# Kernel optimization log

Measured on AMD Instinct MI355X. Metric: run time of the kernel, lower is better.

## Reference

```python
import jax, jax.numpy as jnp
import numpy as np

# norse LIFParameters defaults with v_th overridden to 0.23
DT = 1e-3
TAU_SYN_INV = 200.0   # 1/5e-3
TAU_MEM_INV = 100.0   # 1/1e-2
V_TH = 0.23
ENC_V_TH = 1.0        # encoder uses default LIFParameters (v_th=1.0)
SEQ_LEN = 24
HIDDEN = 256
N_CLASSES = 10


def heaviside(x):
    return (x > 0).astype(x.dtype)


def encode(x):
    """ConstantCurrentLIFEncoder: lif_current_encoder over SEQ_LEN steps. x: [B, F] -> [T, B, F] spikes."""
    def step(v, _):
        v = v + DT * TAU_MEM_INV * (x - v)          # dv = dt*tau_mem_inv*((v_leak - v) + I)
        z = heaviside(v - ENC_V_TH)
        v = (1.0 - z) * v                            # reset to v_reset = 0
        return v, z
    _, zs = jax.lax.scan(step, jnp.zeros_like(x), None, length=SEQ_LEN)
    return zs


def lif_ff_step(inp, v, i):
    """norse lif_feed_forward_step: decay v with old i, decay i, spike, reset, then add input to i."""
    v_dec = v + DT * TAU_MEM_INV * (i - v)           # v_leak = 0
    i_dec = i * (1.0 - DT * TAU_SYN_INV)
    z = heaviside(v_dec - V_TH)
    v_new = (1.0 - z) * v_dec                        # v_reset = 0
    i_new = i_dec + inp
    return z, v_new, i_new


def setup_inputs() -> dict:
    key = jax.random.key(0)
    ks = jax.random.split(key, 8)
    B, F = 4096, 1024
    def lin(k, fan_in, fan_out):
        bound = 1.0 / np.sqrt(fan_in)
        kw, kb = jax.random.split(k)
        W = jax.random.uniform(kw, (fan_out, fan_in), jnp.float32, -bound, bound)
        b = jax.random.uniform(kb, (fan_out,), jnp.float32, -bound, bound)
        return W, b
    x = jax.random.normal(ks[0], (B, F), jnp.float32)
    W1, b1 = lin(ks[1], F, HIDDEN)
    W2, b2 = lin(ks[2], HIDDEN, HIDDEN)
    W3, b3 = lin(ks[3], HIDDEN, HIDDEN)
    Wli = jax.random.normal(ks[4], (N_CLASSES, HIDDEN), jnp.float32) * np.sqrt(2.0 / HIDDEN)
    return {"x": x, "W1": W1, "b1": b1, "W2": W2, "b2": b2, "W3": W3, "b3": b3, "Wli": Wli}


def reference(x, W1, b1, W2, b2, W3, b3, Wli):
    # dropout layers are identity in eval mode
    enc = encode(x)                                   # [T, B, F]
    B = x.shape[0]
    z2 = lambda d: jnp.zeros((B, d), x.dtype)
    carry0 = (z2(HIDDEN), z2(HIDDEN), z2(HIDDEN), z2(HIDDEN), z2(HIDDEN), z2(HIDDEN),
              z2(N_CLASSES), z2(N_CLASSES))
    def step(c, z):
        v1, i1, v2, i2, v3, i3, vo, io = c
        o1, v1, i1 = lif_ff_step(z @ W1.T + b1, v1, i1)
        o2, v2, i2 = lif_ff_step(o1 @ W2.T + b2, v2, i2)
        o2 = o2 + o1                                  # residual
        o3, v3, i3 = lif_ff_step(o2 @ W3.T + b3, v3, i3)
        o3 = o3 + o2                                  # residual
        # LILinearCell li_step: v from old i, i decays then accumulates W @ input (no bias)
        vo = vo + DT * TAU_MEM_INV * (io - vo)
        io = io * (1.0 - DT * TAU_SYN_INV) + o3 @ Wli.T
        return (v1, i1, v2, i2, v3, i3, vo, io), vo
    _, voltages = jax.lax.scan(step, carry0, enc)     # [T, B, n_classes]
    return voltages[-1]                               # decode = last timestep
```

## Files before the change

### kernel.cpp

```cpp
#include <hip/hip_runtime.h>
#include <hip/hip_bf16.h>

#define FEAT   1024
#define HID    256
#define TSTEPS 24
#define NCLS   10

typedef unsigned int u32;
typedef unsigned long long u64;
typedef unsigned short u16;
typedef float v2f __attribute__((ext_vector_type(2)));

constexpr int OFF_W1T  = 0;
constexpr int OFF_W2T  = OFF_W1T + 1025*HID;
constexpr int OFF_W3T  = OFF_W2T + 257*HID;
constexpr int OFF_WLI  = OFF_W3T + 257*HID;
constexpr int OFF_B1   = OFF_WLI + NCLS*HID;
constexpr int OFF_B2   = OFF_B1 + HID;
constexpr int OFF_B3   = OFF_B2 + HID;

struct CoefT { float c[TSTEPS]; };
constexpr CoefT make_coef() {
    CoefT r{};
    double c = 0.0, p9 = 1.0;
    r.c[TSTEPS-1] = 0.0f;
    for (int u = TSTEPS-1; u > 0; u--) {
        c = 0.8 * c + 0.1 * p9;
        p9 *= 0.9;
        r.c[u-1] = (float)c;
    }
    return r;
}
__device__ constexpr CoefT COEF = make_coef();

__device__ __forceinline__ u32 rfl(u32 v) {
    return (u32)__builtin_amdgcn_readfirstlane((int)v);
}

__device__ __forceinline__ u32 detect_bf16(const void* __restrict__ x, u32 lane) {
    float v = __bfloat162float(((const __hip_bfloat16*)x)[lane]);
    u64 bad = __ballot(!(fabsf(v) < 100.0f));
    return bad == 0ull ? 1u : 0u;
}

__device__ __forceinline__ float rd_any(const void* p, int idx, u32 isbf) {
    return isbf ? __bfloat162float(((const __hip_bfloat16*)p)[idx])
                : ((const float*)p)[idx];
}

__device__ __forceinline__ float4 rd4(const void* p, int i, u32 isbf) {
    if (isbf) {
        const u32* q = (const u32*)p;
        u32 a = q[i >> 1], b = q[(i >> 1) + 1];
        float4 r;
        r.x = __uint_as_float(a << 16); r.y = __uint_as_float(a & 0xffff0000u);
        r.z = __uint_as_float(b << 16); r.w = __uint_as_float(b & 0xffff0000u);
        return r;
    }
    return ((const float4*)p)[i >> 2];
}

__global__ __launch_bounds__(256) void prep_k(const void* __restrict__ x,
        const void* W1, const void* W2, const void* W3, const void* Wli,
        const void* b1, const void* b2, const void* b3, float* __restrict__ ws) {
    const u32 isbf = detect_bf16(x, threadIdx.x & 63);
    const u32 t = threadIdx.x;
    int b = blockIdx.x;

    if (b == 384) {
        for (u32 e = t; e < NCLS*HID; e += 256) ws[OFF_WLI + e] = rd_any(Wli, e, isbf);
        ws[OFF_B1 + t] = rd_any(b1, t, isbf);
        ws[OFF_B2 + t] = rd_any(b2, t, isbf);
        ws[OFF_B3 + t] = rd_any(b3, t, isbf);
        ws[OFF_W1T + 1024*HID + t] = 0.f;
        ws[OFF_W2T + 256*HID + t] = 0.f;
        ws[OFF_W3T + 256*HID + t] = 0.f;
        return;
    }

    const void* src; float* dst; int srcW, h0, f0;
    if (b < 256)      { src = W1; dst = ws + OFF_W1T; srcW = FEAT; h0 = (b >> 5) * 32; f0 = (b & 31) * 32; }
    else if (b < 320) { int tb = b - 256; src = W2; dst = ws + OFF_W2T; srcW = HID; h0 = (tb >> 3) * 32; f0 = (tb & 7) * 32; }
    else              { int tb = b - 320; src = W3; dst = ws + OFF_W3T; srcW = HID; h0 = (tb >> 3) * 32; f0 = (tb & 7) * 32; }

    __shared__ float sm[32 * 36];
    {
        u32 r = t >> 3, c4 = (t & 7) * 4;
        float4 w = rd4(src, (h0 + r) * srcW + f0 + c4, isbf);
        *(float4*)&sm[r * 36 + c4] = w;
    }
    __syncthreads();
    {
        u32 f = t >> 3, h4 = (t & 7) * 4;
        float4 o;
        o.x = sm[(h4 + 0) * 36 + f];
        o.y = sm[(h4 + 1) * 36 + f];
        o.z = sm[(h4 + 2) * 36 + f];
        o.w = sm[(h4 + 3) * 36 + f];
        *(float4*)&dst[(size_t)(f0 + f) * HID + h0 + h4] = o;
    }
}

__device__ __forceinline__ u32 mbcnt64(u64 m) {
    return __builtin_amdgcn_mbcnt_hi((u32)(m >> 32),
           __builtin_amdgcn_mbcnt_lo((u32)m, 0u));
}


__device__ __forceinline__ u32 build_listE(u16* list, u32 lm, u32 lane) {
    u32 cnt = (u32)__builtin_popcount(lm);
    u32 pos = 0, n = 0;
    #pragma unroll
    for (int b = 0; b < 5; b++) {
        u64 B = __ballot(((cnt >> b) & 1u) != 0);
        pos += mbcnt64(B) << b;
        n += ((u32)__builtin_popcountll(B)) << b;
    }
    while (lm) {
        u32 j = (u32)__builtin_ctz(lm); lm &= lm - 1;
        list[pos++] = (u16)((lane << 4) + j);
    }
    u32 np = (n + 1u) & ~1u;
    if (lane == 0 && np != n) list[n] = (u16)1024;
    return np;
}

__device__ __forceinline__ u32 build_listZ(u16* list, u32 lm, u32 start, u32 lane) {
    u32 cnt = (u32)__builtin_popcount(lm);
    u64 B0 = __ballot((cnt & 1u) != 0);
    u64 B1 = __ballot((cnt & 2u) != 0);
    u64 B2 = __ballot((cnt & 4u) != 0);
    u32 pos = start + mbcnt64(B0) + 2u*mbcnt64(B1) + 4u*mbcnt64(B2);
    u32 n = start + (u32)__builtin_popcountll(B0) + 2u*(u32)__builtin_popcountll(B1)
          + 4u*(u32)__builtin_popcountll(B2);
    while (lm) {
        u32 j = (u32)__builtin_ctz(lm); lm &= lm - 1;
        list[pos++] = (u16)((lane << 2) + j);
    }
    u32 np = (n + 1u) & ~1u;
    if (lane == 0 && np != n) list[n] = (u16)256;
    return np;
}

#define GADD(AA, BB, V) do { AA += (v2f){(V).x, (V).y}; BB += (v2f){(V).z, (V).w}; } while (0)

__device__ __forceinline__ void gather(v2f& A, v2f& B, const float* __restrict__ Wt,
                                       const u16* __restrict__ list, u32 np, u32 lane16) {
    const char* __restrict__ base = (const char*)Wt;
    u32 c = 0;
    for (; c + 8 <= np; c += 8) {
        uint4 d = *(const uint4*)(list + c);
        u32 w0 = rfl(d.x), w1 = rfl(d.y), w2 = rfl(d.z), w3 = rfl(d.w);
        const float4 v0 = *(const float4*)(base + ((w0 & 0xffffu) << 10) + lane16);
        const float4 v1 = *(const float4*)(base + ((w0 >> 16)     << 10) + lane16);
        const float4 v2 = *(const float4*)(base + ((w1 & 0xffffu) << 10) + lane16);
        const float4 v3 = *(const float4*)(base + ((w1 >> 16)     << 10) + lane16);
        const float4 v4 = *(const float4*)(base + ((w2 & 0xffffu) << 10) + lane16);
        const float4 v5 = *(const float4*)(base + ((w2 >> 16)     << 10) + lane16);
        const float4 v6 = *(const float4*)(base + ((w3 & 0xffffu) << 10) + lane16);
        const float4 v7 = *(const float4*)(base + ((w3 >> 16)     << 10) + lane16);
        GADD(A, B, v0); GADD(A, B, v1); GADD(A, B, v2); GADD(A, B, v3);
        GADD(A, B, v4); GADD(A, B, v5); GADD(A, B, v6); GADD(A, B, v7);
    }
    for (; c < np; c += 2) {
        u32 d = rfl(*(const u32*)(list + c));
        const float4 v0 = *(const float4*)(base + ((d & 0xffffu) << 10) + lane16);
        const float4 v1 = *(const float4*)(base + ((d >> 16)     << 10) + lane16);
        GADD(A, B, v0); GADD(A, B, v1);
    }
}

__device__ __forceinline__ void gather_dual(v2f& A2, v2f& B2, v2f& A3, v2f& B3,
        const float* __restrict__ W2t, const float* __restrict__ W3t,
        const u16* __restrict__ list, u32 np, u32 lane16) {
    const char* __restrict__ p2 = (const char*)W2t;
    const char* __restrict__ p3 = (const char*)W3t;
    u32 c = 0;
    for (; c + 4 <= np; c += 4) {
        uint2 d = *(const uint2*)(list + c);
        u32 w0 = rfl(d.x), w1 = rfl(d.y);
        u32 o0 = (w0 & 0xffffu) << 10, o1 = (w0 >> 16) << 10;
        u32 o2 = (w1 & 0xffffu) << 10, o3 = (w1 >> 16) << 10;
        const float4 a0 = *(const float4*)(p2 + o0 + lane16);
        const float4 a1 = *(const float4*)(p2 + o1 + lane16);
        const float4 a2 = *(const float4*)(p2 + o2 + lane16);
        const float4 a3 = *(const float4*)(p2 + o3 + lane16);
        const float4 c0 = *(const float4*)(p3 + o0 + lane16);
        const float4 c1 = *(const float4*)(p3 + o1 + lane16);
        const float4 c2 = *(const float4*)(p3 + o2 + lane16);
        const float4 c3 = *(const float4*)(p3 + o3 + lane16);
        GADD(A2, B2, a0); GADD(A2, B2, a1); GADD(A2, B2, a2); GADD(A2, B2, a3);
        GADD(A3, B3, c0); GADD(A3, B3, c1); GADD(A3, B3, c2); GADD(A3, B3, c3);
    }
    for (; c < np; c += 2) {
        u32 d = rfl(*(const u32*)(list + c));
        u32 o0 = (d & 0xffffu) << 10, o1 = (d >> 16) << 10;
        const float4 a0 = *(const float4*)(p2 + o0 + lane16);
        const float4 a1 = *(const float4*)(p2 + o1 + lane16);
        const float4 c0 = *(const float4*)(p3 + o0 + lane16);
        const float4 c1 = *(const float4*)(p3 + o1 + lane16);
        GADD(A2, B2, a0); GADD(A2, B2, a1);
        GADD(A3, B3, c0); GADD(A3, B3, c1);
    }
}

__global__ __launch_bounds__(64) void snn_k(const void* __restrict__ xin,
                                            const float* __restrict__ ws,
                                            void* __restrict__ out) {
    const u32 lane = threadIdx.x;
    const int row  = blockIdx.x;
    const u32 lane16 = lane * 16;
    const u32 isbf = detect_bf16(xin, lane);

    const float* __restrict__ W1T = ws + OFF_W1T;
    const float* __restrict__ W2T = ws + OFF_W2T;
    const float* __restrict__ W3T = ws + OFF_W3T;
    const float* __restrict__ WLI = ws + OFF_WLI;

    __shared__ u32 sched[12 * 64];
    __shared__ __align__(16) u16 lE[1032];
    __shared__ __align__(16) u16 lL[520];

    {
        float xv[16];
        if (isbf) {
            const uint4* xp = (const uint4*)((const u16*)xin + (size_t)row*FEAT + lane*16);
            uint4 A = xp[0], B = xp[1];
            u32 w[8] = {A.x, A.y, A.z, A.w, B.x, B.y, B.z, B.w};
            #pragma unroll
            for (int i = 0; i < 8; i++) {
                xv[2*i]   = __uint_as_float(w[i] << 16);
                xv[2*i+1] = __uint_as_float(w[i] & 0xffff0000u);
            }
        } else {
            const float4* xp = (const float4*)((const float*)xin + (size_t)row*FEAT + lane*16);
            float4 A = xp[0], B = xp[1], C = xp[2], D = xp[3];
            float tmp[16] = {A.x,A.y,A.z,A.w,B.x,B.y,B.z,B.w,C.x,C.y,C.z,C.w,D.x,D.y,D.z,D.w};
            #pragma unroll
            for (int i = 0; i < 16; i++) xv[i] = tmp[i];
        }
        u32 smreg[12];
        #pragma unroll
        for (int i = 0; i < 12; i++) smreg[i] = 0;
        #pragma unroll
        for (int j = 0; j < 16; j++) {
            float v = 0.f;
            #pragma unroll
            for (int t = 0; t < TSTEPS; t++) {
                v = v + 0.1f * (xv[j] - v);
                bool z = v > 1.0f;
                v = z ? 0.0f : v;
                if (z) smreg[t >> 1] |= 1u << (((t & 1) << 4) + j);
            }
        }
        #pragma unroll
        for (int i = 0; i < 12; i++) sched[i * 64 + lane] = smreg[i];
    }

    float v1[4], i1[4], v2[4], i2[4], v3[4], i3[4], g[4];
    #pragma unroll
    for (int k = 0; k < 4; k++) {
        v1[k]=0.f; i1[k]=0.f; v2[k]=0.f; i2[k]=0.f; v3[k]=0.f; i3[k]=0.f; g[k]=0.f;
    }
    const u32 lane4 = lane * 4;
    const float4 b1v = *(const float4*)(ws + OFF_B1 + lane4);
    const float4 b2v = *(const float4*)(ws + OFF_B2 + lane4);
    const float4 b3v = *(const float4*)(ws + OFF_B3 + lane4);

    u32 pairreg = 0;
    for (int t = 0; t < TSTEPS; t++) {
        if ((t & 1) == 0) pairreg = sched[(t >> 1) * 64 + lane];
        const u32 lmE = (t & 1) ? (pairreg >> 16) : (pairreg & 0xffffu);

        v2f accA = {b1v.x, b1v.y}, accB = {b1v.z, b1v.w};
        if (__ballot(lmE != 0u)) {
            u32 npE = build_listE(lE, lmE, lane);
            gather(accA, accB, W1T, lE, npE, lane16);
        }
        float a1[4] = {accA.x, accA.y, accB.x, accB.y};

        float o1v[4]; u32 lm1 = 0;
        #pragma unroll
        for (int kk = 0; kk < 4; kk++) {
            float vd = v1[kk] + 0.1f * (i1[kk] - v1[kk]);
            i1[kk] = i1[kk] * 0.8f;
            bool z = vd > 0.23f;
            v1[kk] = z ? 0.0f : vd;
            i1[kk] = i1[kk] + a1[kk];
            o1v[kk] = z ? 1.0f : 0.0f;
            lm1 |= (z ? 1u : 0u) << kk;
        }

        v2f acc2A = {b2v.x, b2v.y}, acc2B = {b2v.z, b2v.w};
        v2f acc3A = {b3v.x, b3v.y}, acc3B = {b3v.z, b3v.w};
        u32 np1 = 0;
        if (__ballot(lm1 != 0u)) {
            np1 = build_listZ(lL, lm1, 0u, lane);
            gather_dual(acc2A, acc2B, acc3A, acc3B, W2T, W3T, lL, np1, lane16);
        }
        float a2[4] = {acc2A.x, acc2A.y, acc2B.x, acc2B.y};

        float o2v[4]; u32 lm2 = 0;
        #pragma unroll
        for (int kk = 0; kk < 4; kk++) {
            float vd = v2[kk] + 0.1f * (i2[kk] - v2[kk]);
            i2[kk] = i2[kk] * 0.8f;
            bool z = vd > 0.23f;
            v2[kk] = z ? 0.0f : vd;
            i2[kk] = i2[kk] + a2[kk];
            o2v[kk] = (z ? 1.0f : 0.0f) + o1v[kk];
            lm2 |= (z ? 1u : 0u) << kk;
        }

        if (__ballot(lm2 != 0u)) {
            u32 np2 = build_listZ(lL, lm2, np1, lane);
            gather(acc3A, acc3B, W3T, lL + np1, np2 - np1, lane16);
        }
        float a3[4] = {acc3A.x, acc3A.y, acc3B.x, acc3B.y};

        const float cf = COEF.c[t];
        #pragma unroll
        for (int kk = 0; kk < 4; kk++) {
            float vd = v3[kk] + 0.1f * (i3[kk] - v3[kk]);
            i3[kk] = i3[kk] * 0.8f;
            bool z = vd > 0.23f;
            v3[kk] = z ? 0.0f : vd;
            i3[kk] = i3[kk] + a3[kk];
            float o3 = (z ? 1.0f : 0.0f) + o2v[kk];
            g[kk] += cf * o3;
        }
    }

    float s[NCLS];
    #pragma unroll
    for (int c = 0; c < NCLS; c++) {
        const float4 w = *(const float4*)(WLI + c*HID + lane4);
        float p = g[0]*w.x + g[1]*w.y + g[2]*w.z + g[3]*w.w;
        #pragma unroll
        for (int d = 32; d > 0; d >>= 1) p += __shfl_xor(p, d, 64);
        s[c] = p;
    }
    if (lane == 0) {
        if (isbf) {
            __hip_bfloat16* o = (__hip_bfloat16*)out + (size_t)row*NCLS;
            #pragma unroll
            for (int c = 0; c < NCLS; c++) o[c] = __float2bfloat16(s[c]);
        } else {
            float* o = (float*)out + (size_t)row*NCLS;
            #pragma unroll
            for (int c = 0; c < NCLS; c++) o[c] = s[c];
        }
    }
}

extern "C" void kernel_launch(void* const* d_in, const int* in_sizes, int n_in,
                              void* d_out, int out_size, void* d_ws, size_t ws_size,
                              hipStream_t stream) {
    const void* x   = d_in[0];
    const void* W1  = d_in[1];
    const void* b1  = d_in[2];
    const void* W2  = d_in[3];
    const void* b2  = d_in[4];
    const void* W3  = d_in[5];
    const void* b3  = d_in[6];
    const void* Wli = d_in[7];
    float* ws = (float*)d_ws;
    const int batch = in_sizes[0] / FEAT;

    prep_k<<<385, 256, 0, stream>>>(x, W1, W2, W3, Wli, b1, b2, b3, ws);
    snn_k<<<batch, 64, 0, stream>>>(x, ws, d_out);
}
```

Measured before the change: 144.1 us.

## Split each batch row across two wavefronts with K-split gathers and LDS reduction

Each block now runs two wavefronts per batch row. Each wave handles half of the input features or hidden spikes (a K-split) and accumulates partial sums over all 256 outputs. The two waves exchange and sum their partials through shared memory with a __syncthreads at each layer, and each wave then owns 2 of the 4 outputs per lane for the LIF state update. The aim is to halve the per-wave serial gather latency and raise parallelism, at the cost of three block barriers per timestep and extra LDS traffic.

Result: slower. 228.3 us (+58.4%).

```diff
diff --git a/kernel.cpp b/kernel.cpp
--- a/kernel.cpp
+++ b/kernel.cpp
@@ -107,35 +107,33 @@
 }
 
 
-__device__ __forceinline__ u32 build_listE(u16* list, u32 lm, u32 lane) {
+__device__ __forceinline__ u32 build_listE8(u16* list, u32 lm, u32 lane, u32 colbase) {
     u32 cnt = (u32)__builtin_popcount(lm);
     u32 pos = 0, n = 0;
     #pragma unroll
-    for (int b = 0; b < 5; b++) {
+    for (int b = 0; b < 4; b++) {
         u64 B = __ballot(((cnt >> b) & 1u) != 0);
         pos += mbcnt64(B) << b;
         n += ((u32)__builtin_popcountll(B)) << b;
     }
     while (lm) {
         u32 j = (u32)__builtin_ctz(lm); lm &= lm - 1;
-        list[pos++] = (u16)((lane << 4) + j);
+        list[pos++] = (u16)(colbase + (lane << 3) + j);
     }
     u32 np = (n + 1u) & ~1u;
     if (lane == 0 && np != n) list[n] = (u16)1024;
     return np;
 }
 
-__device__ __forceinline__ u32 build_listZ(u16* list, u32 lm, u32 start, u32 lane) {
+__device__ __forceinline__ u32 build_listZ2(u16* list, u32 lm, u32 start, u32 lane, u32 kbase) {
     u32 cnt = (u32)__builtin_popcount(lm);
     u64 B0 = __ballot((cnt & 1u) != 0);
     u64 B1 = __ballot((cnt & 2u) != 0);
-    u64 B2 = __ballot((cnt & 4u) != 0);
-    u32 pos = start + mbcnt64(B0) + 2u*mbcnt64(B1) + 4u*mbcnt64(B2);
-    u32 n = start + (u32)__builtin_popcountll(B0) + 2u*(u32)__builtin_popcountll(B1)
-          + 4u*(u32)__builtin_popcountll(B2);
+    u32 pos = start + mbcnt64(B0) + 2u*mbcnt64(B1);
+    u32 n = start + (u32)__builtin_popcountll(B0) + 2u*(u32)__builtin_popcountll(B1);
     while (lm) {
         u32 j = (u32)__builtin_ctz(lm); lm &= lm - 1;
-        list[pos++] = (u16)((lane << 2) + j);
+        list[pos++] = (u16)((lane << 2) + kbase + j);
     }
     u32 np = (n + 1u) & ~1u;
     if (lane == 0 && np != n) list[n] = (u16)256;
@@ -204,12 +202,15 @@
     }
 }
 
-__global__ __launch_bounds__(64) void snn_k(const void* __restrict__ xin,
-                                            const float* __restrict__ ws,
-                                            void* __restrict__ out) {
-    const u32 lane = threadIdx.x;
+__global__ __launch_bounds__(128, 8) void snn_k(const void* __restrict__ xin,
+                                                const float* __restrict__ ws,
+                                                void* __restrict__ out) {
+    const u32 tid  = threadIdx.x;
+    const u32 w    = tid >> 6;
+    const u32 lane = tid & 63;
     const int row  = blockIdx.x;
     const u32 lane16 = lane * 16;
+    const u32 k0 = w << 1;
     const u32 isbf = detect_bf16(xin, lane);
 
     const float* __restrict__ W1T = ws + OFF_W1T;
@@ -217,71 +218,82 @@
     const float* __restrict__ W3T = ws + OFF_W3T;
     const float* __restrict__ WLI = ws + OFF_WLI;
 
-    __shared__ u32 sched[12 * 64];
-    __shared__ __align__(16) u16 lE[1032];
-    __shared__ __align__(16) u16 lL[520];
+    __shared__ u32 sched[6 * 128];
+    __shared__ __align__(16) u16 lE[2][512];
+    __shared__ __align__(16) u16 lL[2][264];
+    __shared__ v2f exb[3][2][64];
+    __shared__ float redsm[2][NCLS];
 
     {
-        float xv[16];
+        float xv[8];
         if (isbf) {
-            const uint4* xp = (const uint4*)((const u16*)xin + (size_t)row*FEAT + lane*16);
-            uint4 A = xp[0], B = xp[1];
-            u32 w[8] = {A.x, A.y, A.z, A.w, B.x, B.y, B.z, B.w};
+            const u16* xb = (const u16*)xin + (size_t)row * FEAT;
+            uint4 A = *(const uint4*)(xb + tid * 8);
+            u32 wd[4] = {A.x, A.y, A.z, A.w};
             #pragma unroll
-            for (int i = 0; i < 8; i++) {
-                xv[2*i]   = __uint_as_float(w[i] << 16);
-                xv[2*i+1] = __uint_as_float(w[i] & 0xffff0000u);
+            for (int i = 0; i < 4; i++) {
+                xv[2*i]   = __uint_as_float(wd[i] << 16);
+                xv[2*i+1] = __uint_as_float(wd[i] & 0xffff0000u);
             }
         } else {
-            const float4* xp = (const float4*)((const float*)xin + (size_t)row*FEAT + lane*16);
-            float4 A = xp[0], B = xp[1], C = xp[2], D = xp[3];
-            float tmp[16] = {A.x,A.y,A.z,A.w,B.x,B.y,B.z,B.w,C.x,C.y,C.z,C.w,D.x,D.y,D.z,D.w};
-            #pragma unroll
-            for (int i = 0; i < 16; i++) xv[i] = tmp[i];
-        }
-        u32 smreg[12];
-        #pragma unroll
-        for (int i = 0; i < 12; i++) smreg[i] = 0;
-        #pragma unroll
-        for (int j = 0; j < 16; j++) {
+            const float* xf = (const float*)xin + (size_t)row * FEAT;
+            float4 A = ((const float4*)xf)[tid * 2];
+            float4 B = ((const float4*)xf)[tid * 2 + 1];
+            xv[0]=A.x; xv[1]=A.y; xv[2]=A.z; xv[3]=A.w;
+            xv[4]=B.x; xv[5]=B.y; xv[6]=B.z; xv[7]=B.w;
+        }
+        u32 smreg[6];
+        #pragma unroll
+        for (int i = 0; i < 6; i++) smreg[i] = 0;
+        #pragma unroll
+        for (int j = 0; j < 8; j++) {
             float v = 0.f;
             #pragma unroll
             for (int t = 0; t < TSTEPS; t++) {
                 v = v + 0.1f * (xv[j] - v);
                 bool z = v > 1.0f;
                 v = z ? 0.0f : v;
-                if (z) smreg[t >> 1] |= 1u << (((t & 1) << 4) + j);
+                if (z) smreg[t >> 2] |= 1u << (((t & 3) << 3) + j);
             }
         }
         #pragma unroll
-        for (int i = 0; i < 12; i++) sched[i * 64 + lane] = smreg[i];
-    }
-
-    float v1[4], i1[4], v2[4], i2[4], v3[4], i3[4], g[4];
+        for (int i = 0; i < 6; i++) sched[i * 128 + tid] = smreg[i];
+    }
+
+    float v1[2], i1[2], v2_[2], i2[2], v3[2], i3[2], g[2];
     #pragma unroll
-    for (int k = 0; k < 4; k++) {
-        v1[k]=0.f; i1[k]=0.f; v2[k]=0.f; i2[k]=0.f; v3[k]=0.f; i3[k]=0.f; g[k]=0.f;
+    for (int k = 0; k < 2; k++) {
+        v1[k]=0.f; i1[k]=0.f; v2_[k]=0.f; i2[k]=0.f; v3[k]=0.f; i3[k]=0.f; g[k]=0.f;
     }
     const u32 lane4 = lane * 4;
-    const float4 b1v = *(const float4*)(ws + OFF_B1 + lane4);
-    const float4 b2v = *(const float4*)(ws + OFF_B2 + lane4);
-    const float4 b3v = *(const float4*)(ws + OFF_B3 + lane4);
-
-    u32 pairreg = 0;
+    float4 b1v = *(const float4*)(ws + OFF_B1 + lane4);
+    float4 b2v = *(const float4*)(ws + OFF_B2 + lane4);
+    float4 b3v = *(const float4*)(ws + OFF_B3 + lane4);
+    if (w) {
+        b1v = make_float4(0.f,0.f,0.f,0.f);
+        b2v = make_float4(0.f,0.f,0.f,0.f);
+        b3v = make_float4(0.f,0.f,0.f,0.f);
+    }
+    const u32 colbaseE = w << 9;
+
+    u32 curw = 0;
     for (int t = 0; t < TSTEPS; t++) {
-        if ((t & 1) == 0) pairreg = sched[(t >> 1) * 64 + lane];
-        const u32 lmE = (t & 1) ? (pairreg >> 16) : (pairreg & 0xffffu);
+        if ((t & 3) == 0) curw = sched[(t >> 2) * 128 + tid];
+        const u32 lmE = (curw >> ((t & 3) << 3)) & 0xffu;
 
         v2f accA = {b1v.x, b1v.y}, accB = {b1v.z, b1v.w};
         if (__ballot(lmE != 0u)) {
-            u32 npE = build_listE(lE, lmE, lane);
-            gather(accA, accB, W1T, lE, npE, lane16);
-        }
-        float a1[4] = {accA.x, accA.y, accB.x, accB.y};
-
-        float o1v[4]; u32 lm1 = 0;
-        #pragma unroll
-        for (int kk = 0; kk < 4; kk++) {
+            u32 npE = build_listE8(lE[w], lmE, lane, colbaseE);
+            gather(accA, accB, W1T, lE[w], npE, lane16);
+        }
+        exb[0][w][lane] = w ? accA : accB;
+        __syncthreads();
+        v2f own1 = (w ? accB : accA) + exb[0][w ^ 1][lane];
+
+        float a1[2] = {own1.x, own1.y};
+        float o1v[2]; u32 lm1 = 0;
+        #pragma unroll
+        for (int kk = 0; kk < 2; kk++) {
             float vd = v1[kk] + 0.1f * (i1[kk] - v1[kk]);
             i1[kk] = i1[kk] * 0.8f;
             bool z = vd > 0.23f;
@@ -295,32 +307,38 @@
         v2f acc3A = {b3v.x, b3v.y}, acc3B = {b3v.z, b3v.w};
         u32 np1 = 0;
         if (__ballot(lm1 != 0u)) {
-            np1 = build_listZ(lL, lm1, 0u, lane);
-            gather_dual(acc2A, acc2B, acc3A, acc3B, W2T, W3T, lL, np1, lane16);
-        }
-        float a2[4] = {acc2A.x, acc2A.y, acc2B.x, acc2B.y};
-
-        float o2v[4]; u32 lm2 = 0;
-        #pragma unroll
-        for (int kk = 0; kk < 4; kk++) {
-            float vd = v2[kk] + 0.1f * (i2[kk] - v2[kk]);
+            np1 = build_listZ2(lL[w], lm1, 0u, lane, k0);
+            gather_dual(acc2A, acc2B, acc3A, acc3B, W2T, W3T, lL[w], np1, lane16);
+        }
+        exb[1][w][lane] = w ? acc2A : acc2B;
+        __syncthreads();
+        v2f own2 = (w ? acc2B : acc2A) + exb[1][w ^ 1][lane];
+
+        float a2[2] = {own2.x, own2.y};
+        float o2v[2]; u32 lm2 = 0;
+        #pragma unroll
+        for (int kk = 0; kk < 2; kk++) {
+            float vd = v2_[kk] + 0.1f * (i2[kk] - v2_[kk]);
             i2[kk] = i2[kk] * 0.8f;
             bool z = vd > 0.23f;
-            v2[kk] = z ? 0.0f : vd;
+            v2_[kk] = z ? 0.0f : vd;
             i2[kk] = i2[kk] + a2[kk];
             o2v[kk] = (z ? 1.0f : 0.0f) + o1v[kk];
             lm2 |= (z ? 1u : 0u) << kk;
         }
 
         if (__ballot(lm2 != 0u)) {
-            u32 np2 = build_listZ(lL, lm2, np1, lane);
-            gather(acc3A, acc3B, W3T, lL + np1, np2 - np1, lane16);
-        }
-        float a3[4] = {acc3A.x, acc3A.y, acc3B.x, acc3B.y};
-
+            u32 np2 = build_listZ2(lL[w], lm2, np1, lane, k0);
+            gather(acc3A, acc3B, W3T, lL[w] + np1, np2 - np1, lane16);
+        }
+        exb[2][w][lane] = w ? acc3A : acc3B;
+        __syncthreads();
+        v2f own3 = (w ? acc3B : acc3A) + exb[2][w ^ 1][lane];
+
+        float a3[2] = {own3.x, own3.y};
         const float cf = COEF.c[t];
         #pragma unroll
-        for (int kk = 0; kk < 4; kk++) {
+        for (int kk = 0; kk < 2; kk++) {
             float vd = v3[kk] + 0.1f * (i3[kk] - v3[kk]);
             i3[kk] = i3[kk] * 0.8f;
             bool z = vd > 0.23f;
@@ -334,21 +352,26 @@
     float s[NCLS];
     #pragma unroll
     for (int c = 0; c < NCLS; c++) {
-        const float4 w = *(const float4*)(WLI + c*HID + lane4);
-        float p = g[0]*w.x + g[1]*w.y + g[2]*w.z + g[3]*w.w;
+        const float2 wv = *(const float2*)(WLI + c * HID + lane4 + k0);
+        float p = g[0] * wv.x + g[1] * wv.y;
         #pragma unroll
         for (int d = 32; d > 0; d >>= 1) p += __shfl_xor(p, d, 64);
         s[c] = p;
     }
     if (lane == 0) {
+        #pragma unroll
+        for (int c = 0; c < NCLS; c++) redsm[w][c] = s[c];
+    }
+    __syncthreads();
+    if (tid == 0) {
         if (isbf) {
-            __hip_bfloat16* o = (__hip_bfloat16*)out + (size_t)row*NCLS;
+            __hip_bfloat16* o = (__hip_bfloat16*)out + (size_t)row * NCLS;
             #pragma unroll
-            for (int c = 0; c < NCLS; c++) o[c] = __float2bfloat16(s[c]);
+            for (int c = 0; c < NCLS; c++) o[c] = __float2bfloat16(redsm[0][c] + redsm[1][c]);
         } else {
-            float* o = (float*)out + (size_t)row*NCLS;
+            float* o = (float*)out + (size_t)row * NCLS;
             #pragma unroll
-            for (int c = 0; c < NCLS; c++) o[c] = s[c];
+            for (int c = 0; c < NCLS; c++) o[c] = redsm[0][c] + redsm[1][c];
         }
     }
 }
@@ -368,5 +391,5 @@
     const int batch = in_sizes[0] / FEAT;
 
     prep_k<<<385, 256, 0, stream>>>(x, W1, W2, W3, Wli, b1, b2, b3, ws);
-    snn_k<<<batch, 64, 0, stream>>>(x, ws, d_out);
-}
+    snn_k<<<batch, 128, 0, stream>>>(x, ws, d_out);
+}
```
